# Optimization experiments

Measured on AMD Instinct MI355X. Metric: run time of the kernel, lower is better.

The kernel has to match this reference:

```python
import jax, jax.numpy as jnp
import numpy as np

N_NODES = 100000
N_EDGES = 3200000
IN_DIM = 11
HID = 32


def setup_inputs() -> dict:
    key = jax.random.key(0)
    ks = jax.random.split(key, 12)
    inp = {
        "x": jax.random.normal(ks[0], (N_NODES, IN_DIM), dtype=jnp.float32),
        "edge_index": jax.random.randint(ks[1], (2, N_EDGES), 0, N_NODES, dtype=jnp.int32),
        "batch": jnp.zeros((N_NODES,), dtype=jnp.int32),
        # GCNConv layer 1 (11 -> 32)
        "W1": jax.random.normal(ks[2], (IN_DIM, HID), dtype=jnp.float32) / np.sqrt(IN_DIM),
        "b1": jnp.zeros((HID,), dtype=jnp.float32),
        # GCNConv layer 2 (32 -> 32)
        "W2": jax.random.normal(ks[3], (HID, HID), dtype=jnp.float32) / np.sqrt(HID),
        "b2": jnp.zeros((HID,), dtype=jnp.float32),
        # output MLP: 32 -> 16 -> 1
        "Wo1": jax.random.normal(ks[4], (HID, HID // 2), dtype=jnp.float32) / np.sqrt(HID),
        "bo1": jnp.zeros((HID // 2,), dtype=jnp.float32),
        "Wo2": jax.random.normal(ks[5], (HID // 2, 1), dtype=jnp.float32) / np.sqrt(HID // 2),
        "bo2": jnp.zeros((1,), dtype=jnp.float32),
    }
    return inp


def _gcn_norm(edge_index, n_nodes):
    # Add self-loops and compute symmetric normalization (PyG GCNConv default).
    loops = jnp.arange(n_nodes, dtype=edge_index.dtype)
    src = jnp.concatenate([edge_index[0], loops])
    dst = jnp.concatenate([edge_index[1], loops])
    ones = jnp.ones_like(dst, dtype=jnp.float32)
    deg = jax.ops.segment_sum(ones, dst, num_segments=n_nodes)  # degree of A+I on target side
    dinv = jax.lax.rsqrt(deg)  # deg >= 1 thanks to self-loops
    norm = dinv[src] * dinv[dst]  # [E+N]
    return src, dst, norm


def _gcn_conv(x, W, b, src, dst, norm, n_nodes):
    xw = x @ W                                   # transform first (small dim)
    msg = norm[:, None] * xw[src]                # gather + scale  [E+N, H]
    agg = jax.ops.segment_sum(msg, dst, num_segments=n_nodes)  # scatter-add
    return agg + b


def reference(x, edge_index, batch, W1, b1, W2, b2, Wo1, bo1, Wo2, bo2):
    n = x.shape[0]
    src, dst, norm = _gcn_norm(edge_index, n)
    h = jax.nn.relu(_gcn_conv(x, W1, b1, src, dst, norm, n))
    # F.dropout(training=self.training) is identity in eval mode
    h = jax.nn.relu(_gcn_conv(h, W2, b2, src, dst, norm, n))
    h = jax.nn.elu(h @ Wo1 + bo1)
    out = h @ Wo2 + bo2
    return out.squeeze(-1)  # [N]
```

## Files before the change

### kernel.cpp

```cpp
#include <hip/hip_runtime.h>
#include <hip/hip_fp16.h>
#include <math.h>

#define N_NODES 100000
#define N_EDGES 3200000
#define IN_DIM 11
#define HID 32
#define HID2 16
#define SCHUNK 100352
#define BINSHIFT 8
#define BINSZ 256
#define NB 391
#define CHUNK 8192

__global__ __launch_bounds__(1024) void k_hist(const int* __restrict__ ei,
                                               int* __restrict__ bincnt) {
    __shared__ int h[NB];
    for (int i = threadIdx.x; i < NB; i += 1024) h[i] = 0;
    __syncthreads();
    int b0 = blockIdx.x * CHUNK;
    int e1 = b0 + CHUNK; if (e1 > N_EDGES) e1 = N_EDGES;
    for (int e = b0 + threadIdx.x; e < e1; e += 1024)
        atomicAdd(&h[ei[N_EDGES + e] >> BINSHIFT], 1);
    __syncthreads();
    for (int i = threadIdx.x; i < NB; i += 1024)
        if (h[i]) atomicAdd(&bincnt[i], h[i]);
}

__global__ __launch_bounds__(1024) void k_binscatter(const int* __restrict__ ei,
                                                     const int* __restrict__ bincnt,
                                                     int* __restrict__ bincur,
                                                     unsigned* __restrict__ binbuf) {
    __shared__ int pre[NB];
    __shared__ int h[NB];
    __shared__ int base[NB];
    __shared__ int tmp[512];
    int tid = threadIdx.x;
    int v = (tid < NB) ? bincnt[tid] : 0;
    if (tid < 512) tmp[tid] = v;
    __syncthreads();
    for (int off = 1; off < 512; off <<= 1) {
        int t = (tid < 512 && tid >= off) ? tmp[tid - off] : 0;
        __syncthreads();
        if (tid < 512) tmp[tid] += t;
        __syncthreads();
    }
    if (tid < NB) pre[tid] = tmp[tid] - v;
    for (int i = tid; i < NB; i += 1024) h[i] = 0;
    __syncthreads();
    int b0 = blockIdx.x * CHUNK;
    int e1 = b0 + CHUNK; if (e1 > N_EDGES) e1 = N_EDGES;
    for (int e = b0 + tid; e < e1; e += 1024)
        atomicAdd(&h[ei[N_EDGES + e] >> BINSHIFT], 1);
    __syncthreads();
    for (int i = tid; i < NB; i += 1024) {
        int c = h[i];
        if (c) base[i] = pre[i] + atomicAdd(&bincur[i], c);
        h[i] = 0;
    }
    __syncthreads();
    for (int e = b0 + tid; e < e1; e += 1024) {
        int d = ei[N_EDGES + e];
        int s = ei[e];
        int b = d >> BINSHIFT;
        int p = base[b] + atomicAdd(&h[b], 1);
        binbuf[p] = (unsigned)s | ((unsigned)(d & (BINSZ - 1)) << 17);
    }
}

__global__ __launch_bounds__(1024) void k_binfill(const unsigned* __restrict__ binbuf,
                                                  const int* __restrict__ bincnt,
                                                  int* __restrict__ rowstart,
                                                  float* __restrict__ dinv,
                                                  int* __restrict__ csr_src) {
    int b = blockIdx.x;
    int tid = threadIdx.x;
    __shared__ int tmp[512];
    __shared__ int cnt[BINSZ];
    __shared__ int rloc[BINSZ];
    __shared__ int cur[BINSZ];
    int v = (tid < 512 && tid < b) ? bincnt[tid] : 0;
    if (tid < 512) tmp[tid] = v;
    __syncthreads();
    for (int off = 256; off >= 1; off >>= 1) {
        if (tid < off) tmp[tid] += tmp[tid + off];
        __syncthreads();
    }
    int ebeg = tmp[0];
    int eend = ebeg + bincnt[b];
    __syncthreads();
    if (tid < BINSZ) cnt[tid] = 0;
    __syncthreads();
    for (int e = ebeg + tid; e < eend; e += 1024)
        atomicAdd(&cnt[binbuf[e] >> 17], 1);
    __syncthreads();
    int c = (tid < BINSZ) ? cnt[tid] : 0;
    if (tid < BINSZ) tmp[tid] = c;
    __syncthreads();
    for (int off = 1; off < BINSZ; off <<= 1) {
        int t = (tid < BINSZ && tid >= off) ? tmp[tid - off] : 0;
        __syncthreads();
        if (tid < BINSZ) tmp[tid] += t;
        __syncthreads();
    }
    if (tid < BINSZ) {
        rloc[tid] = tmp[tid] - c;
        cur[tid] = 0;
        int node = b * BINSZ + tid;
        if (node < N_NODES) {
            rowstart[node] = ebeg + rloc[tid];
            dinv[node] = rsqrtf((float)c + 1.0f);
        }
    }
    if (b == 0 && tid == 0) rowstart[N_NODES] = N_EDGES;
    __syncthreads();
    for (int e = ebeg + tid; e < eend; e += 1024) {
        unsigned vv = binbuf[e];
        int dl = vv >> 17;
        int s = (int)(vv & 0x1FFFFu);
        int p = ebeg + rloc[dl] + atomicAdd(&cur[dl], 1);
        csr_src[p] = s;
    }
}

__global__ void k_xw1(const float* __restrict__ x, const float* __restrict__ W1,
                      const float* __restrict__ dinv, __half* __restrict__ xwh) {
    int t = blockIdx.x * blockDim.x + threadIdx.x;
    int node = t >> 5;
    int j = t & 31;
    __shared__ float sW[IN_DIM * HID];
    __shared__ float sx[8 * IN_DIM];
    for (int i = threadIdx.x; i < IN_DIM * HID; i += 256) sW[i] = W1[i];
    int base = blockIdx.x * 8;
    if (threadIdx.x < 8 * IN_DIM) sx[threadIdx.x] = x[base * IN_DIM + threadIdx.x];
    __syncthreads();
    int ln = node - base;
    float acc = 0.0f;
#pragma unroll
    for (int k = 0; k < IN_DIM; ++k)
        acc += sx[ln * IN_DIM + k] * sW[k * HID + j];
    xwh[t] = __float2half(dinv[node] * acc);
}

__device__ __forceinline__ float edge_accum(int beg, int end, int j,
                                            const int* __restrict__ csr_src,
                                            const __half* __restrict__ xwh) {
    float acc = 0.0f;
    int e = beg;
    for (; e + 16 <= end; e += 16) {
        int s[16];
#pragma unroll
        for (int u = 0; u < 16; ++u) s[u] = csr_src[e + u];
        float xv[16];
#pragma unroll
        for (int u = 0; u < 16; ++u) xv[u] = __half2float(xwh[s[u] * HID + j]);
        float a0 = ((xv[0] + xv[1]) + (xv[2] + xv[3])) + ((xv[4] + xv[5]) + (xv[6] + xv[7]));
        float a1 = ((xv[8] + xv[9]) + (xv[10] + xv[11])) + ((xv[12] + xv[13]) + (xv[14] + xv[15]));
        acc += a0 + a1;
    }
    if (e + 8 <= end) {
        int s0 = csr_src[e],     s1 = csr_src[e + 1], s2 = csr_src[e + 2], s3 = csr_src[e + 3];
        int s4 = csr_src[e + 4], s5 = csr_src[e + 5], s6 = csr_src[e + 6], s7 = csr_src[e + 7];
        float x0 = __half2float(xwh[s0 * HID + j]);
        float x1 = __half2float(xwh[s1 * HID + j]);
        float x2 = __half2float(xwh[s2 * HID + j]);
        float x3 = __half2float(xwh[s3 * HID + j]);
        float x4 = __half2float(xwh[s4 * HID + j]);
        float x5 = __half2float(xwh[s5 * HID + j]);
        float x6 = __half2float(xwh[s6 * HID + j]);
        float x7 = __half2float(xwh[s7 * HID + j]);
        acc += ((x0 + x1) + (x2 + x3)) + ((x4 + x5) + (x6 + x7));
        e += 8;
    }
    for (; e + 2 <= end; e += 2) {
        int s0 = csr_src[e], s1 = csr_src[e + 1];
        acc += __half2float(xwh[s0 * HID + j]) + __half2float(xwh[s1 * HID + j]);
    }
    for (; e < end; ++e)
        acc += __half2float(xwh[csr_src[e] * HID + j]);
    return acc;
}

__global__ __launch_bounds__(256) void k_gather_xw2(const int* __restrict__ rowstart,
                                                    const float* __restrict__ dinv,
                                                    const int* __restrict__ csr_src,
                                                    const __half* __restrict__ xwh1,
                                                    const float* __restrict__ b1,
                                                    const float* __restrict__ W2,
                                                    __half* __restrict__ xwh2) {
    __shared__ float sW2[HID * HID];
    __shared__ float sH[8 * 33];
    for (int i = threadIdx.x; i < HID * HID; i += 256) sW2[i] = W2[i];
    __syncthreads();

    int ln = threadIdx.x >> 5;
    int node = blockIdx.x * 8 + ln;
    int j = threadIdx.x & 31;
    float acc = edge_accum(rowstart[node], rowstart[node + 1], j, csr_src, xwh1);
    float dd = dinv[node];
    float hv = dd * (acc + __half2float(xwh1[node * HID + j])) + b1[j];
    sH[ln * 33 + j] = hv > 0.0f ? hv : 0.0f;
    __syncthreads();

    float a2 = 0.0f;
#pragma unroll
    for (int k = 0; k < HID; ++k) a2 += sH[ln * 33 + k] * sW2[k * HID + j];
    xwh2[node * HID + j] = __float2half(dd * a2);
}

__global__ __launch_bounds__(256) void k_gather_mlp(const int* __restrict__ rowstart,
                                                    const float* __restrict__ dinv,
                                                    const int* __restrict__ csr_src,
                                                    const __half* __restrict__ xwh,
                                                    const float* __restrict__ b2,
                                                    const float* __restrict__ Wo1,
                                                    const float* __restrict__ bo1,
                                                    const float* __restrict__ Wo2,
                                                    const float* __restrict__ bo2,
                                                    float* __restrict__ out) {
    __shared__ float sW1[HID * HID2];
    __shared__ float sb1[HID2];
    __shared__ float sW2[HID2];
    __shared__ float sb2[HID];
    __shared__ float sH[8 * 33];
    for (int i = threadIdx.x; i < HID * HID2; i += 256) sW1[i] = Wo1[i];
    if (threadIdx.x < HID2) {
        sb1[threadIdx.x] = bo1[threadIdx.x];
        sW2[threadIdx.x] = Wo2[threadIdx.x];
    }
    if (threadIdx.x < HID) sb2[threadIdx.x] = b2[threadIdx.x];
    __syncthreads();

    int ln = threadIdx.x >> 5;
    int node = blockIdx.x * 8 + ln;
    int j = threadIdx.x & 31;
    float acc = edge_accum(rowstart[node], rowstart[node + 1], j, csr_src, xwh);
    float dd = dinv[node];
    float hv = dd * (acc + __half2float(xwh[node * HID + j])) + sb2[j];
    sH[ln * 33 + j] = hv > 0.0f ? hv : 0.0f;
    __syncthreads();

    float val = 0.0f;
    if (j < HID2) {
        float a = sb1[j];
#pragma unroll
        for (int k = 0; k < HID; ++k) a += sH[ln * 33 + k] * sW1[k * HID2 + j];
        a = a > 0.0f ? a : (expf(a) - 1.0f);
        val = a * sW2[j];
    }
#pragma unroll
    for (int d = 16; d >= 1; d >>= 1) val += __shfl_down(val, d, 32);
    if (j == 0) out[node] = val + bo2[0];
}

extern "C" void kernel_launch(void* const* d_in, const int* in_sizes, int n_in,
                              void* d_out, int out_size, void* d_ws, size_t ws_size,
                              hipStream_t stream) {
    const float* x   = (const float*)d_in[0];
    const int*   ei  = (const int*)d_in[1];
    const float* W1  = (const float*)d_in[3];
    const float* b1  = (const float*)d_in[4];
    const float* W2  = (const float*)d_in[5];
    const float* b2  = (const float*)d_in[6];
    const float* Wo1 = (const float*)d_in[7];
    const float* bo1 = (const float*)d_in[8];
    const float* Wo2 = (const float*)d_in[9];
    const float* bo2 = (const float*)d_in[10];
    float* out = (float*)d_out;

    int*      bincnt   = (int*)d_ws;
    int*      bincur   = bincnt + 512;
    int*      rowstart = bincur + 512;
    float*    dinv     = (float*)(rowstart + SCHUNK);
    int*      csr_src  = (int*)(dinv + SCHUNK);
    unsigned* binbuf   = (unsigned*)(csr_src + N_EDGES);
    __half*   XWH1     = (__half*)(binbuf + N_EDGES);
    __half*   XWH2     = XWH1 + (size_t)N_NODES * HID;

    const int BT = 256;
    int gNH  = (N_NODES * HID + BT - 1) / BT;
    int gC   = (N_EDGES + CHUNK - 1) / CHUNK;
    int gG   = N_NODES / 8;

    hipMemsetAsync(bincnt, 0, 1024 * sizeof(int), stream);
    k_hist      <<<gC, 1024, 0, stream>>>(ei, bincnt);
    k_binscatter<<<gC, 1024, 0, stream>>>(ei, bincnt, bincur, binbuf);
    k_binfill   <<<NB, 1024, 0, stream>>>(binbuf, bincnt, rowstart, dinv, csr_src);

    k_xw1<<<gNH, BT, 0, stream>>>(x, W1, dinv, XWH1);
    k_gather_xw2<<<gG, BT, 0, stream>>>(rowstart, dinv, csr_src, XWH1, b1, W2, XWH2);

    k_gather_mlp<<<gG, BT, 0, stream>>>(rowstart, dinv, csr_src, XWH2,
                                        b2, Wo1, bo1, Wo2, bo2, out);
}
```

Before: 275.5 us.

## Vectorize CSR gather: each lane loads 8 halves per edge, reduce via shuffles

The per-node edge aggregation now splits the 32 lanes into 8 edge slots by 4 feature quarters. Each lane issues 16-byte loads of 8 fp16 features for a different edge instead of one 2-byte load per feature per edge, with partial sums combined by xor shuffles and staged through shared memory. This cuts the number of gather load instructions and widens each memory transaction, at the cost of more registers, extra shuffles and an additional shared-memory staging step.

```diff
diff --git a/kernel.cpp b/kernel.cpp
--- a/kernel.cpp
+++ b/kernel.cpp
@@ -142,43 +142,59 @@
     xwh[t] = __float2half(dinv[node] * acc);
 }
 
-__device__ __forceinline__ float edge_accum(int beg, int end, int j,
+__device__ __forceinline__ void accum8(float* __restrict__ acc, const uint4 v) {
+    float2 f0 = __half22float2(*(const __half2*)&v.x);
+    float2 f1 = __half22float2(*(const __half2*)&v.y);
+    float2 f2 = __half22float2(*(const __half2*)&v.z);
+    float2 f3 = __half22float2(*(const __half2*)&v.w);
+    acc[0] += f0.x; acc[1] += f0.y;
+    acc[2] += f1.x; acc[3] += f1.y;
+    acc[4] += f2.x; acc[5] += f2.y;
+    acc[6] += f3.x; acc[7] += f3.y;
+}
+
+__device__ __forceinline__ void edge_accum8(int beg, int end, int q, int oj,
                                             const int* __restrict__ csr_src,
-                                            const __half* __restrict__ xwh) {
-    float acc = 0.0f;
+                                            const __half* __restrict__ xwh,
+                                            float* __restrict__ acc) {
+#pragma unroll
+    for (int k = 0; k < 8; ++k) acc[k] = 0.0f;
     int e = beg;
-    for (; e + 16 <= end; e += 16) {
-        int s[16];
-#pragma unroll
-        for (int u = 0; u < 16; ++u) s[u] = csr_src[e + u];
-        float xv[16];
-#pragma unroll
-        for (int u = 0; u < 16; ++u) xv[u] = __half2float(xwh[s[u] * HID + j]);
-        float a0 = ((xv[0] + xv[1]) + (xv[2] + xv[3])) + ((xv[4] + xv[5]) + (xv[6] + xv[7]));
-        float a1 = ((xv[8] + xv[9]) + (xv[10] + xv[11])) + ((xv[12] + xv[13]) + (xv[14] + xv[15]));
-        acc += a0 + a1;
+    for (; e + 32 <= end; e += 32) {
+        int s0 = csr_src[e + q];
+        int s1 = csr_src[e + 8 + q];
+        int s2 = csr_src[e + 16 + q];
+        int s3 = csr_src[e + 24 + q];
+        uint4 v0 = *(const uint4*)(xwh + ((s0 << 5) | oj));
+        uint4 v1 = *(const uint4*)(xwh + ((s1 << 5) | oj));
+        uint4 v2 = *(const uint4*)(xwh + ((s2 << 5) | oj));
+        uint4 v3 = *(const uint4*)(xwh + ((s3 << 5) | oj));
+        accum8(acc, v0); accum8(acc, v1); accum8(acc, v2); accum8(acc, v3);
+    }
+    if (e + 16 <= end) {
+        int s0 = csr_src[e + q];
+        int s1 = csr_src[e + 8 + q];
+        uint4 v0 = *(const uint4*)(xwh + ((s0 << 5) | oj));
+        uint4 v1 = *(const uint4*)(xwh + ((s1 << 5) | oj));
+        accum8(acc, v0); accum8(acc, v1);
+        e += 16;
     }
     if (e + 8 <= end) {
-        int s0 = csr_src[e],     s1 = csr_src[e + 1], s2 = csr_src[e + 2], s3 = csr_src[e + 3];
-        int s4 = csr_src[e + 4], s5 = csr_src[e + 5], s6 = csr_src[e + 6], s7 = csr_src[e + 7];
-        float x0 = __half2float(xwh[s0 * HID + j]);
-        float x1 = __half2float(xwh[s1 * HID + j]);
-        float x2 = __half2float(xwh[s2 * HID + j]);
-        float x3 = __half2float(xwh[s3 * HID + j]);
-        float x4 = __half2float(xwh[s4 * HID + j]);
-        float x5 = __half2float(xwh[s5 * HID + j]);
-        float x6 = __half2float(xwh[s6 * HID + j]);
-        float x7 = __half2float(xwh[s7 * HID + j]);
-        acc += ((x0 + x1) + (x2 + x3)) + ((x4 + x5) + (x6 + x7));
+        int s0 = csr_src[e + q];
+        uint4 v0 = *(const uint4*)(xwh + ((s0 << 5) | oj));
+        accum8(acc, v0);
         e += 8;
     }
-    for (; e + 2 <= end; e += 2) {
-        int s0 = csr_src[e], s1 = csr_src[e + 1];
-        acc += __half2float(xwh[s0 * HID + j]) + __half2float(xwh[s1 * HID + j]);
-    }
-    for (; e < end; ++e)
-        acc += __half2float(xwh[csr_src[e] * HID + j]);
-    return acc;
+    if (e + q < end) {
+        int s0 = csr_src[e + q];
+        uint4 v0 = *(const uint4*)(xwh + ((s0 << 5) | oj));
+        accum8(acc, v0);
+    }
+#pragma unroll
+    for (int m = 4; m <= 16; m <<= 1) {
+#pragma unroll
+        for (int k = 0; k < 8; ++k) acc[k] += __shfl_xor(acc[k], m);
+    }
 }
 
 __global__ __launch_bounds__(256) void k_gather_xw2(const int* __restrict__ rowstart,
@@ -189,22 +205,33 @@
                                                     const float* __restrict__ W2,
                                                     __half* __restrict__ xwh2) {
     __shared__ float sW2[HID * HID];
-    __shared__ float sH[8 * 33];
+    __shared__ float sA[8][33];
+    __shared__ float sH[8][33];
     for (int i = threadIdx.x; i < HID * HID; i += 256) sW2[i] = W2[i];
-    __syncthreads();
 
     int ln = threadIdx.x >> 5;
     int node = blockIdx.x * 8 + ln;
-    int j = threadIdx.x & 31;
-    float acc = edge_accum(rowstart[node], rowstart[node + 1], j, csr_src, xwh1);
+    int l = threadIdx.x & 31;
+    int q = l >> 2;
+    int oj = (l & 3) << 3;
+
+    float acc[8];
+    edge_accum8(rowstart[node], rowstart[node + 1], q, oj, csr_src, xwh1, acc);
+    if (q == 0) {
+#pragma unroll
+        for (int k = 0; k < 8; ++k) sA[ln][oj + k] = acc[k];
+    }
+    __syncthreads();
+
+    int j = l;
     float dd = dinv[node];
-    float hv = dd * (acc + __half2float(xwh1[node * HID + j])) + b1[j];
-    sH[ln * 33 + j] = hv > 0.0f ? hv : 0.0f;
+    float hv = dd * (sA[ln][j] + __half2float(xwh1[node * HID + j])) + b1[j];
+    sH[ln][j] = hv > 0.0f ? hv : 0.0f;
     __syncthreads();
 
     float a2 = 0.0f;
 #pragma unroll
-    for (int k = 0; k < HID; ++k) a2 += sH[ln * 33 + k] * sW2[k * HID + j];
+    for (int k = 0; k < HID; ++k) a2 += sH[ln][k] * sW2[k * HID + j];
     xwh2[node * HID + j] = __float2half(dd * a2);
 }
 
@@ -220,33 +247,44 @@
                                                     float* __restrict__ out) {
     __shared__ float sW1[HID * HID2];
     __shared__ float sb1[HID2];
-    __shared__ float sW2[HID2];
+    __shared__ float sW2v[HID2];
     __shared__ float sb2[HID];
-    __shared__ float sH[8 * 33];
+    __shared__ float sA[8][33];
+    __shared__ float sH[8][33];
     for (int i = threadIdx.x; i < HID * HID2; i += 256) sW1[i] = Wo1[i];
     if (threadIdx.x < HID2) {
         sb1[threadIdx.x] = bo1[threadIdx.x];
-        sW2[threadIdx.x] = Wo2[threadIdx.x];
+        sW2v[threadIdx.x] = Wo2[threadIdx.x];
     }
     if (threadIdx.x < HID) sb2[threadIdx.x] = b2[threadIdx.x];
-    __syncthreads();
 
     int ln = threadIdx.x >> 5;
     int node = blockIdx.x * 8 + ln;
-    int j = threadIdx.x & 31;
-    float acc = edge_accum(rowstart[node], rowstart[node + 1], j, csr_src, xwh);
+    int l = threadIdx.x & 31;
+    int q = l >> 2;
+    int oj = (l & 3) << 3;
+
+    float acc[8];
+    edge_accum8(rowstart[node], rowstart[node + 1], q, oj, csr_src, xwh, acc);
+    if (q == 0) {
+#pragma unroll
+        for (int k = 0; k < 8; ++k) sA[ln][oj + k] = acc[k];
+    }
+    __syncthreads();
+
+    int j = l;
     float dd = dinv[node];
-    float hv = dd * (acc + __half2float(xwh[node * HID + j])) + sb2[j];
-    sH[ln * 33 + j] = hv > 0.0f ? hv : 0.0f;
+    float hv = dd * (sA[ln][j] + __half2float(xwh[node * HID + j])) + sb2[j];
+    sH[ln][j] = hv > 0.0f ? hv : 0.0f;
     __syncthreads();
 
     float val = 0.0f;
     if (j < HID2) {
         float a = sb1[j];
 #pragma unroll
-        for (int k = 0; k < HID; ++k) a += sH[ln * 33 + k] * sW1[k * HID2 + j];
+        for (int k = 0; k < HID; ++k) a += sH[ln][k] * sW1[k * HID2 + j];
         a = a > 0.0f ? a : (expf(a) - 1.0f);
-        val = a * sW2[j];
+        val = a * sW2v[j];
     }
 #pragma unroll
     for (int d = 16; d >= 1; d >>= 1) val += __shfl_down(val, d, 32);
```

Measured after the change: 260.1 us. 1.06x faster.
